# Optimization experiments

Measured on AMD Instinct MI355X. Metric: run time of the kernel, lower is better.

## Reference

```python
import jax, jax.numpy as jnp
import numpy as np

SR = 44100.0
BS, NT, SEQ = 2, 16, 262144
REV_N, TAPS = 65536, 1023

EQ_R = [(-12., 12.), (20., 2000.), (0.1, 5.0),
        (-12., 12.), (80., 2000.), (0.1, 5.0),
        (-12., 12.), (2000., 8000.), (0.1, 5.0),
        (-12., 12.), (8000., 12000.), (0.1, 5.0),
        (-12., 12.), (12000., 21050.), (0.1, 5.0),
        (-12., 12.), (6000., 21050.), (0.1, 5.0)]
COMP_R = [(-60., 0.), (1., 10.), (5., 250.), (10., 250.), (3., 12.), (0., 6.)]
TRACK_R = np.array([(-48., 48.)] + EQ_R + COMP_R + [(-80., 12.), (0., 1.)], np.float32)
MASTER_R = np.array([(-48., 48.)] + EQ_R + COMP_R + [(-48., 48.)], np.float32)


def _pow2(n):
    return 1 << int(np.ceil(np.log2(n)))


def _denorm(p, r):
    lo = jnp.asarray(r[:, 0])
    hi = jnp.asarray(r[:, 1])
    return p * (hi - lo) + lo


def _biquad(g_db, fc, q, ftype):
    # RBJ cookbook biquads, coefficients normalized by a0
    A = 10.0 ** (g_db / 40.0)
    w0 = 2.0 * np.pi * (fc / SR)
    al = jnp.sin(w0) / (2.0 * q)
    c = jnp.cos(w0)
    sA = jnp.sqrt(A)
    if ftype == 'low_shelf':
        b0 = A * ((A + 1) - (A - 1) * c + 2 * sA * al)
        b1 = 2 * A * ((A - 1) - (A + 1) * c)
        b2 = A * ((A + 1) - (A - 1) * c - 2 * sA * al)
        a0 = (A + 1) + (A - 1) * c + 2 * sA * al
        a1 = -2 * ((A - 1) + (A + 1) * c)
        a2 = (A + 1) + (A - 1) * c - 2 * sA * al
    elif ftype == 'high_shelf':
        b0 = A * ((A + 1) + (A - 1) * c + 2 * sA * al)
        b1 = -2 * A * ((A - 1) + (A + 1) * c)
        b2 = A * ((A + 1) + (A - 1) * c - 2 * sA * al)
        a0 = (A + 1) - (A - 1) * c + 2 * sA * al
        a1 = 2 * ((A - 1) - (A + 1) * c)
        a2 = (A + 1) - (A - 1) * c - 2 * sA * al
    else:  # peaking
        b0 = 1 + al * A
        b1 = -2 * c
        b2 = 1 - al * A
        a0 = 1 + al / A
        a1 = -2 * c
        a2 = 1 - al / A
    b = jnp.stack([b0, b1, b2], -1) / a0[..., None]
    a = jnp.stack([a0, a1, a2], -1) / a0[..., None]
    return b, a


def _apply_eq(x, p):
    # 6-section cascaded biquad EQ applied via frequency sampling (as dasp_pytorch does).
    # x: (..., S); p: (..., 18) broadcastable with x's leading dims.
    S = x.shape[-1]
    nfft = _pow2(2 * S - 1)
    nf = nfft // 2 + 1
    w = jnp.arange(nf, dtype=jnp.float32) * (2.0 * np.pi / nfft)
    z1 = jnp.exp(-1j * w)
    z2 = z1 * z1
    H = jnp.ones((nf,), jnp.complex64)
    for k, ftype in enumerate(['low_shelf', 'peaking', 'peaking', 'peaking', 'peaking', 'high_shelf']):
        b, a = _biquad(p[..., 3 * k], p[..., 3 * k + 1], p[..., 3 * k + 2], ftype)
        num = b[..., 0:1] + b[..., 1:2] * z1 + b[..., 2:3] * z2
        den = a[..., 0:1] + a[..., 1:2] * z1 + a[..., 2:3] * z2
        H = H * (num / den)
    X = jnp.fft.rfft(x, nfft)
    return jnp.fft.irfft(X * H, nfft)[..., :S].astype(x.dtype)


def _apply_comp(x, p, lookahead):
    # soft-knee compressor; gain smoothed by one-pole (attack) via frequency sampling.
    S = x.shape[-1]
    nfft = _pow2(2 * S - 1)
    nf = nfft // 2 + 1
    th, ratio, at_ms, rel_ms, knee, makeup = [p[..., i:i + 1] for i in range(6)]
    x_db = 20.0 * jnp.log10(jnp.maximum(jnp.abs(x), 1e-8))
    d = x_db - th
    x_sc = jnp.where(2.0 * d < -knee, x_db,
                     jnp.where(2.0 * jnp.abs(d) <= knee,
                               x_db + (1.0 / ratio - 1.0) * (d + knee / 2.0) ** 2 / (2.0 * knee),
                               th + d / ratio))
    g_c = x_sc - x_db  # gain reduction in dB (<= 0)
    alpha = jnp.exp(-jnp.log(9.0) / (SR * at_ms * 1e-3))  # (..., 1)
    w = jnp.arange(nf, dtype=jnp.float32) * (2.0 * np.pi / nfft)
    H = (1.0 - alpha) / (1.0 - alpha * jnp.exp(-1j * w))
    g_s = jnp.fft.irfft(jnp.fft.rfft(g_c, nfft) * H, nfft)[..., :S]
    if lookahead > 0:
        tail = jnp.repeat(g_s[..., -1:], lookahead, axis=-1)
        g_s = jnp.concatenate([g_s[..., lookahead:], tail], axis=-1)
    return (x * 10.0 ** ((g_s + makeup) / 20.0)).astype(x.dtype)


def _reverb(x, noise, fb, gains, decays, mix):
    # noise-shaped reverberation: 12 octave-band filtered noise bursts with
    # exponential decays summed into an IR, FFT-convolved with x, wet/dry mix.
    S = x.shape[-1]
    nL = _pow2(REV_N + TAPS - 1)
    filt = jnp.fft.irfft(jnp.fft.rfft(noise, nL) * jnp.fft.rfft(fb, nL), nL)
    filt = filt[..., TAPS - 1:TAPS - 1 + REV_N]  # (bs, 2, 12, REV_N) 'valid' part
    t = jnp.linspace(0.0, 1.0, REV_N)
    dec = decays * 10.0 + 1.0  # (bs, 12)
    env = jnp.exp(-dec[:, None, :, None] * t)
    ir = (filt * env * gains[:, None, :, None]).mean(axis=2)  # (bs, 2, REV_N)
    n2 = _pow2(S + REV_N - 1)
    wet = jnp.fft.irfft(jnp.fft.rfft(x, n2) * jnp.fft.rfft(ir, n2), n2)[..., :S]
    m = mix[:, None, None]
    return (1.0 - m) * x + m * wet


def _firwin_lp(numtaps, fc, fs):
    n = np.arange(numtaps) - (numtaps - 1) / 2.0
    h = (2.0 * fc / fs) * np.sinc(2.0 * fc / fs * n)
    h = h * np.hamming(numtaps)
    return h / h.sum()


def _octave_fb():
    centers = [31.5, 63., 125., 250., 500., 1000., 2000., 4000., 8000., 16000.]
    nyq = SR / 2.0
    filts = [_firwin_lp(TAPS, 22.3, SR)]  # lowpass below lowest octave
    for fc in centers:
        f1 = fc / np.sqrt(2.0)
        f2 = min(fc * np.sqrt(2.0), 0.999 * nyq)
        filts.append(_firwin_lp(TAPS, f2, SR) - _firwin_lp(TAPS, f1, SR))
    hp = -_firwin_lp(TAPS, 18000.0, SR)
    hp[(TAPS - 1) // 2] += 1.0  # highpass = delta - lowpass
    filts.append(hp)
    return np.stack(filts).astype(np.float32)  # (12, TAPS)


def _forward(tracks, track_params, fx_bus_params, master_bus_params, reverb_noise, fb):
    tpd = _denorm(track_params, TRACK_R)    # (bs, NT, 27)
    mpd = _denorm(master_bus_params, MASTER_R)  # (bs, 26)
    fxp = fx_bus_params  # reverb ranges are (0,1): denorm is identity

    x = tracks * 10.0 ** (tpd[..., 0:1] / 20.0)          # input fader
    x = _apply_eq(x, tpd[..., 1:19])                      # 6-band parametric EQ
    x = _apply_comp(x, tpd[..., 19:25], 2048)             # compressor, lookahead 2048

    theta = tpd[..., 26] * (np.pi / 2)                    # constant-power panner
    gl = jnp.sqrt(((np.pi / 2) - theta) * (2.0 / np.pi) * jnp.cos(theta))
    gr = jnp.sqrt(theta * (2.0 / np.pi) * jnp.sin(theta))
    panned = jnp.stack([x * gl[..., None], x * gr[..., None]], axis=1)  # (bs, 2, NT, S)

    master = panned.sum(axis=2)                           # (bs, 2, S)
    send = 10.0 ** (tpd[..., 25] / 20.0)                  # fx bus sends
    fx_in = (panned * send[:, None, :, None]).sum(axis=2)
    master = master + _reverb(fx_in, reverb_noise, fb, fxp[:, :12], fxp[:, 12:24], fxp[:, 24])

    master = master * 10.0 ** (mpd[:, 0, None, None] / 20.0)   # master input fader
    master = _apply_eq(master, mpd[:, None, 1:19])
    master = _apply_comp(master, mpd[:, None, 19:25], 1024)
    master = master * 10.0 ** (mpd[:, 25, None, None] / 20.0)  # output fader
    return panned, master


def setup_inputs() -> dict:
    key = jax.random.key(0)
    k = jax.random.split(key, 5)
    tracks = 0.1 * jax.random.normal(k[0], (BS, NT, SEQ), jnp.float32)
    track_params = jax.random.uniform(k[1], (BS, NT, 27), jnp.float32)
    fx_bus_params = jax.random.uniform(k[2], (BS, 25), jnp.float32)
    master_bus_params = jax.random.uniform(k[3], (BS, 26), jnp.float32)
    reverb_noise = jax.random.normal(k[4], (BS, 2, 12, REV_N + TAPS - 1), jnp.float32)
    fb = jnp.asarray(_octave_fb())
    return {'tracks': tracks, 'track_params': track_params, 'fx_bus_params': fx_bus_params,
            'master_bus_params': master_bus_params, 'reverb_noise': reverb_noise, 'fb': fb}


def reference(tracks, track_params, fx_bus_params, master_bus_params, reverb_noise, fb):
    return _forward(tracks, track_params, fx_bus_params, master_bus_params, reverb_noise, fb)
```

## Files before the change

### kernel.cpp

```cpp
#include <hip/hip_runtime.h>

#define DEVFN __device__ __forceinline__

constexpr int SEQ = 262144;
constexpr int REV_N = 65536;
constexpr int TAPS = 1023;
constexpr int NOISE_LEN = REV_N + TAPS - 1;

constexpr int NS_T = 32, L_T = 128, C_T = 2048;
constexpr int NS_M = 4,  L_M = 64,  C_M = 4096;
constexpr int LA_T = 2048, LA_M = 1024;

constexpr int OUT_MASTER_OFF = 16777216;

constexpr int PADX = 65552;
constexpr int XBL  = 327744;
constexpr int IRPAD = 4096;
constexpr int IRL  = 73728;
constexpr int PADN = 2016;
constexpr int XNL  = 68640;
constexpr int FPAD = 2048;
constexpr int FBL  = 4160;

#define C_DB  0.16609640474436813f
#define C_LOG 6.0205999132796239f
#define PI_D  3.14159265358979323846

typedef __attribute__((ext_vector_type(8)))  short short8v;
typedef __attribute__((ext_vector_type(16))) float f32x16;

struct SigP {
  float g_in;
  float cb0[6], cb1[6], cb2[6], ca1[6], ca2[6];
  float alpha, oma;
  float th, invr, knee, makeup;
  float g_out;
  float gl, gr, send;
};

constexpr size_t OFF_X   = 0;
constexpr size_t OFF_Y   = 33554432;
constexpr size_t OFF_FX  = 67108864;
constexpr size_t OFF_M0  = 71303168;
constexpr size_t OFF_FILT = OFF_X;
constexpr size_t OFF_IR   = OFF_X + 12582912;
constexpr size_t OFF_XM   = OFF_X + 16777216;
constexpr size_t OFF_M1   = OFF_Y;
constexpr size_t OFF_WP   = OFF_Y + 4194304;
constexpr size_t OFF_XB   = OFF_WP + 16777216;
constexpr size_t OFF_IR2  = OFF_XB + (size_t)4*XBL*2;
constexpr size_t OFF_XBN  = 58720256;
constexpr size_t OFF_FBV  = 65536000;
constexpr size_t OFF_E12 = OFF_FX;
constexpr size_t OFF_I12 = OFF_FX + 3145728;
constexpr size_t OFF_E1  = OFF_FX + 6291456;
constexpr size_t OFF_I1  = OFF_FX + 6553600;
constexpr size_t OFF_GL  = 75497472;
constexpr size_t OFF_PT  = OFF_GL + 1024;
constexpr size_t OFF_PM  = OFF_PT + 32*sizeof(SigP);
constexpr size_t OFF_ALT = (OFF_PM + 4*sizeof(SigP) + 7) & ~(size_t)7;
constexpr size_t OFF_ALM = OFF_ALT + 32*8;
constexpr size_t OFF_AT  = (OFF_ALM + 4*8 + 15) & ~(size_t)15;
constexpr size_t OFF_AM  = OFF_AT + 18432;

DEVFN int pq(int i){ return i + ((i >> 5) << 2); }
DEVFN int pqb(int i){ return i + ((i >> 5) << 3); }

DEVFN unsigned short f2bf(float f){
  unsigned int u = __float_as_uint(f);
  unsigned int r = (u + 0x7fffu + ((u >> 16) & 1u)) >> 16;
  return (unsigned short)r;
}
DEVFN float bf2f(unsigned short h){ return __uint_as_float(((unsigned int)h) << 16); }

DEVFN double dn(float p, double lo, double hi){ return (double)p*(hi-lo)+lo; }

__device__ void mk_sig(const float* p, int L, bool is_master,
                       SigP* sp, float* Tf, double* aL)
{
  const double flo[6] = {20.,80.,2000.,8000.,12000.,6000.};
  const double fhi[6] = {2000.,2000.,8000.,12000.,21050.,21050.};
  double gdb = dn(p[0], -48., 48.);
  sp->g_in = (float)exp2(gdb * 0.16609640474436813);
  double db0[6],db1[6],db2[6],da1[6],da2[6];
  for (int k=0;k<6;k++){
    double g  = dn(p[1+3*k], -12., 12.);
    double fc = dn(p[2+3*k], flo[k], fhi[k]);
    double q  = dn(p[3+3*k], 0.1, 5.0);
    double A  = pow(10.0, g/40.0);
    double w0 = 2.0*PI_D*(fc/44100.0);
    double al = sin(w0)/(2.0*q), co = cos(w0), sA = sqrt(A);
    double b0,b1,b2,a0,a1,a2;
    if (k==0){
      b0 = A*((A+1.0) - (A-1.0)*co + 2.0*sA*al);
      b1 = 2.0*A*((A-1.0) - (A+1.0)*co);
      b2 = A*((A+1.0) - (A-1.0)*co - 2.0*sA*al);
      a0 = (A+1.0) + (A-1.0)*co + 2.0*sA*al;
      a1 = -2.0*((A-1.0) + (A+1.0)*co);
      a2 = (A+1.0) + (A-1.0)*co - 2.0*sA*al;
    } else if (k==5){
      b0 = A*((A+1.0) + (A-1.0)*co + 2.0*sA*al);
      b1 = -2.0*A*((A-1.0) + (A+1.0)*co);
      b2 = A*((A+1.0) + (A-1.0)*co - 2.0*sA*al);
      a0 = (A+1.0) - (A-1.0)*co + 2.0*sA*al;
      a1 = 2.0*((A-1.0) - (A+1.0)*co);
      a2 = (A+1.0) - (A-1.0)*co - 2.0*sA*al;
    } else {
      b0 = 1.0 + al*A; b1 = -2.0*co; b2 = 1.0 - al*A;
      a0 = 1.0 + al/A; a1 = -2.0*co; a2 = 1.0 - al/A;
    }
    double ia0 = 1.0/a0;
    db0[k]=b0*ia0; db1[k]=b1*ia0; db2[k]=b2*ia0; da1[k]=a1*ia0; da2[k]=a2*ia0;
    sp->cb0[k]=(float)db0[k]; sp->cb1[k]=(float)db1[k]; sp->cb2[k]=(float)db2[k];
    sp->ca1[k]=(float)da1[k]; sp->ca2[k]=(float)da2[k];
  }
  for (int i=0;i<12;i++){
    double st[12]; for (int r=0;r<12;r++) st[r]=0.0; st[i]=1.0;
    double ns[12];
    double yprev=0.0, pm1=0.0, pm2=0.0;
    for (int k=0;k<6;k++){
      double yk = db0[k]*yprev + db1[k]*pm1 + db2[k]*pm2 - da1[k]*st[2*k] - da2[k]*st[2*k+1];
      ns[2*k]=yk; ns[2*k+1]=st[2*k];
      pm1=st[2*k]; pm2=st[2*k+1];
      yprev=yk;
    }
    for (int r=0;r<12;r++) Tf[r*12+i]=(float)ns[r];
  }
  double th    = dn(p[19], -60., 0.);
  double ratio = dn(p[20], 1., 10.);
  double at    = dn(p[21], 5., 250.);
  double knee  = dn(p[23], 3., 12.);
  double mkup  = dn(p[24], 0., 6.);
  double alpha = exp(-log(9.0)/(44100.0*at*0.001));
  sp->alpha=(float)alpha; sp->oma=(float)(1.0-alpha);
  sp->th=(float)th; sp->invr=(float)(1.0/ratio); sp->knee=(float)knee; sp->makeup=(float)mkup;
  *aL = pow(alpha, (double)L);
  if (is_master){
    sp->g_out = (float)exp2(dn(p[25],-48.,48.)*0.16609640474436813);
    sp->gl=0.f; sp->gr=0.f; sp->send=0.f;
  } else {
    sp->g_out = 1.f;
    sp->send = (float)exp2(dn(p[25],-80.,12.)*0.16609640474436813);
    double th2 = dn(p[26],0.,1.)*(PI_D/2.0);
    sp->gl = (float)sqrt((PI_D/2.0-th2)*(2.0/PI_D)*cos(th2));
    sp->gr = (float)sqrt(th2*(2.0/PI_D)*sin(th2));
  }
}

__global__ __launch_bounds__(64) void k_params(const float* __restrict__ tp, const float* __restrict__ mp,
    SigP* Pt, SigP* Pm, float* AT, float* AM, double* aLt, double* aLm)
{
  int i = threadIdx.x;
  if (i < 32)       mk_sig(tp + i*27, L_T, false, &Pt[i], AT + i*144, &aLt[i]);
  else if (i < 36){ int j=i-32; mk_sig(mp + (j>>1)*26, L_M, true, &Pm[j], AM + j*144, &aLm[j]); }
}

__global__ __launch_bounds__(64) void k_power(float* __restrict__ Ab, int lg)
{
  __shared__ float Ma[144], Mb[144];
  int sig = blockIdx.x, t = threadIdx.x;
  float* A = Ab + (size_t)sig*144;
  for (int idx=t; idx<144; idx+=64) Ma[idx]=A[idx];
  __syncthreads();
  int cur=0;
  for (int j=0;j<lg;j++){
    const float* src = cur? Mb:Ma;
    float* dst = cur? Ma:Mb;
    for (int idx=t; idx<144; idx+=64){
      int r=idx/12, cc=idx-r*12;
      float v=0.f;
      #pragma unroll
      for (int m=0;m<12;m++) v = fmaf(src[r*12+m], src[m*12+cc], v);
      dst[idx]=v;
    }
    __syncthreads();
    cur^=1;
  }
  const float* fin = cur? Mb:Ma;
  for (int idx=t; idx<144; idx+=64) A[idx]=fin[idx];
}

DEVFN float comp_gc(float y, float th, float invr, float kn){
  float av  = fmaxf(fabsf(y), 1e-8f);
  float xdb = C_LOG * __builtin_log2f(av);
  float d   = xdb - th;
  float w = (2.f*d < -kn) ? 0.f
          : ((2.f*fabsf(d) <= kn) ? (d+0.5f*kn)*(d+0.5f*kn)/(2.f*kn) : d);
  return (invr-1.f)*w;
}

__global__ __launch_bounds__(256) void k_eqA12(const float* __restrict__ in, const SigP* __restrict__ P,
    float* __restrict__ E12, int C, int L)
{
  int tid = blockIdx.x*256 + threadIdx.x;
  int sig = tid / C, c = tid - sig*C;
  const SigP* sp = P + sig;
  float B0[6],B1[6],B2[6],A1[6],A2[6];
  float g = sp->g_in;
  #pragma unroll
  for (int k=0;k<6;k++){
    float gg = (k==0)? g : 1.f;
    B0[k]=sp->cb0[k]*gg; B1[k]=sp->cb1[k]*gg; B2[k]=sp->cb2[k]*gg;
    A1[k]=sp->ca1[k];    A2[k]=sp->ca2[k];
  }
  const float* xp = in + (size_t)sig*SEQ + (size_t)c*L;
  float xm1=0.f, xm2=0.f;
  if (c){ xm1=xp[-1]; xm2=xp[-2]; }
  float s[12];
  #pragma unroll
  for (int r=0;r<12;r++) s[r]=0.f;
  for (int i=0;i<L;i+=4){
    float4 v = *(const float4*)(xp+i);
    #pragma unroll
    for (int u4=0;u4<4;u4++){
      float u = (u4==0)?v.x:(u4==1)?v.y:(u4==2)?v.z:v.w;
      float yprev=u, pm1=xm1, pm2=xm2;
      float ny[6];
      #pragma unroll
      for (int k=0;k<6;k++){
        float t0 = fmaf(B0[k],yprev, fmaf(B1[k],pm1, fmaf(B2[k],pm2, -A2[k]*s[2*k+1])));
        float yk = fmaf(-A1[k], s[2*k], t0);
        ny[k]=yk;
        pm1=s[2*k]; pm2=s[2*k+1];
        yprev=yk;
      }
      #pragma unroll
      for (int k=0;k<6;k++){ s[2*k+1]=s[2*k]; s[2*k]=ny[k]; }
      xm2=xm1; xm1=u;
    }
  }
  float* ep = E12 + (size_t)tid*12;
  #pragma unroll
  for (int r=0;r<12;r++) ep[r]=s[r];
}

__global__ __launch_bounds__(64) void k_scan12(const float* __restrict__ E, float* __restrict__ I,
    const float* __restrict__ Ab, int C, int Q, int lgQ)
{
  __shared__ float As[144], Pa[144], Pb[144];
  __shared__ float seg[64][12], ini[64][12];
  __shared__ float scur[12], stmp[12];
  int sig = blockIdx.x, t = threadIdx.x;
  const float* Asig = Ab + (size_t)sig*144;
  for (int idx=t; idx<144; idx+=64) As[idx]=Asig[idx];
  __syncthreads();
  const float* dp = E + ((size_t)sig*C + (size_t)t*Q)*12;
  float s[12];
  #pragma unroll
  for (int r=0;r<12;r++) s[r]=0.f;
  for (int j=0;j<Q;j++){
    const float* d = dp + j*12;
    float ns[12];
    #pragma unroll
    for (int r=0;r<12;r++){
      float v = d[r];
      #pragma unroll
      for (int cc=0;cc<12;cc++) v = fmaf(As[r*12+cc], s[cc], v);
      ns[r]=v;
    }
    #pragma unroll
    for (int r=0;r<12;r++) s[r]=ns[r];
  }
  #pragma unroll
  for (int r=0;r<12;r++) seg[t][r]=s[r];
  for (int idx=t; idx<144; idx+=64) Pa[idx]=As[idx];
  __syncthreads();
  int cur=0;
  for (int j=0;j<lgQ;j++){
    const float* src = cur? Pb:Pa;
    float* dst = cur? Pa:Pb;
    for (int idx=t; idx<144; idx+=64){
      int r=idx/12, cc=idx-r*12;
      float v=0.f;
      #pragma unroll
      for (int m=0;m<12;m++) v = fmaf(src[r*12+m], src[m*12+cc], v);
      dst[idx]=v;
    }
    __syncthreads();
    cur^=1;
  }
  const float* AQ = cur? Pb:Pa;
  if (t<12) scur[t]=0.f;
  __syncthreads();
  for (int u=0;u<64;u++){
    if (t<12){
      ini[u][t]=scur[t];
      float v = seg[u][t];
      #pragma unroll
      for (int cc=0;cc<12;cc++) v = fmaf(AQ[t*12+cc], scur[cc], v);
      stmp[t]=v;
    }
    __syncthreads();
    if (t<12) scur[t]=stmp[t];
    __syncthreads();
  }
  #pragma unroll
  for (int r=0;r<12;r++) s[r]=ini[t][r];
  float* op = I + ((size_t)sig*C + (size_t)t*Q)*12;
  for (int j=0;j<Q;j++){
    float* o = op + j*12;
    #pragma unroll
    for (int r=0;r<12;r++) o[r]=s[r];
    const float* d = dp + j*12;
    float ns[12];
    #pragma unroll
    for (int r=0;r<12;r++){
      float v = d[r];
      #pragma unroll
      for (int cc=0;cc<12;cc++) v = fmaf(As[r*12+cc], s[cc], v);
      ns[r]=v;
    }
    #pragma unroll
    for (int r=0;r<12;r++) s[r]=ns[r];
  }
}

__global__ __launch_bounds__(64) void k_scan1p(const float* __restrict__ endst, float* __restrict__ inits,
    const double* __restrict__ aL, int C, int Q, int lgQ)
{
  __shared__ double ag[64], ins[64];
  int sig = blockIdx.x; int t = threadIdx.x;
  double a = aL[sig];
  const float* dp = endst + (size_t)sig*C + (size_t)t*Q;
  double e=0.0;
  for (int j=0;j<Q;j++) e = a*e + (double)dp[j];
  ag[t]=e;
  __syncthreads();
  if (t == 0){
    double p=a;
    for (int j=0;j<lgQ;j++) p = p*p;
    double s=0.0;
    for (int u=0;u<64;u++){
      ins[u]=s;
      s = p*s + ag[u];
    }
  }
  __syncthreads();
  double s = ins[t];
  float* op = inits + (size_t)sig*C + (size_t)t*Q;
  for (int j=0;j<Q;j++){ op[j]=(float)s; s = a*s + (double)dp[j]; }
}

__global__ __launch_bounds__(256) void k_eqC12(const float* __restrict__ in, float* __restrict__ yout,
    const SigP* __restrict__ P, const float* __restrict__ I12, float* __restrict__ E1, int C, int L)
{
  int tid = blockIdx.x*256 + threadIdx.x;
  int sig = tid / C, c = tid - sig*C;
  const SigP* sp = P + sig;
  float B0[6],B1[6],B2[6],A1[6],A2[6];
  float g = sp->g_in;
  #pragma unroll
  for (int k=0;k<6;k++){
    float gg = (k==0)? g : 1.f;
    B0[k]=sp->cb0[k]*gg; B1[k]=sp->cb1[k]*gg; B2[k]=sp->cb2[k]*gg;
    A1[k]=sp->ca1[k];    A2[k]=sp->ca2[k];
  }
  float al=sp->alpha, oma=sp->oma, th=sp->th, invr=sp->invr, kn=sp->knee;
  size_t base = (size_t)sig*SEQ + (size_t)c*L;
  const float* xp = in + base;
  float* op = yout + base;
  float xm1=0.f, xm2=0.f;
  if (c){ xm1=xp[-1]; xm2=xp[-2]; }
  const float* ip = I12 + (size_t)tid*12;
  float s[12];
  #pragma unroll
  for (int r=0;r<12;r++) s[r]=ip[r];
  float gacc=0.f;
  for (int i=0;i<L;i+=4){
    float4 v = *(const float4*)(xp+i);
    float4 o;
    #pragma unroll
    for (int u4=0;u4<4;u4++){
      float u = (u4==0)?v.x:(u4==1)?v.y:(u4==2)?v.z:v.w;
      float yprev=u, pm1=xm1, pm2=xm2;
      float ny[6];
      #pragma unroll
      for (int k=0;k<6;k++){
        float t0 = fmaf(B0[k],yprev, fmaf(B1[k],pm1, fmaf(B2[k],pm2, -A2[k]*s[2*k+1])));
        float yk = fmaf(-A1[k], s[2*k], t0);
        ny[k]=yk;
        pm1=s[2*k]; pm2=s[2*k+1];
        yprev=yk;
      }
      #pragma unroll
      for (int k=0;k<6;k++){ s[2*k+1]=s[2*k]; s[2*k]=ny[k]; }
      xm2=xm1; xm1=u;
      float y5 = ny[5];
      if (u4==0) o.x=y5; else if (u4==1) o.y=y5; else if (u4==2) o.z=y5; else o.w=y5;
      gacc = fmaf(al, gacc, oma*comp_gc(y5,th,invr,kn));
    }
    *(float4*)(op+i) = o;
  }
  E1[tid]=gacc;
}

__global__ __launch_bounds__(256) void k_smoothcomp(const float* __restrict__ yin,
    const SigP* __restrict__ P, const float* __restrict__ inits1, float* __restrict__ gslast,
    float* __restrict__ outp, int C, int L, int lac)
{
  int tid = blockIdx.x*256 + threadIdx.x;
  int sig = tid / C, c = tid - sig*C;
  const SigP* sp = P + sig;
  float al=sp->alpha, oma=sp->oma, th=sp->th, invr=sp->invr, kn=sp->knee;
  float mk=sp->makeup, go=sp->g_out;
  size_t base = (size_t)sig*SEQ + (size_t)c*L;
  const float* xp = yin + base;
  bool wr = (c >= lac);
  size_t ob = wr ? (base - (size_t)lac*L) : 0;
  const float* yp = yin + ob;
  float* op = outp + ob;
  float gsv = inits1[tid];
  for (int i=0;i<L;i+=4){
    float4 v = *(const float4*)(xp+i);
    float4 gf;
    gsv = fmaf(al, gsv, oma*comp_gc(v.x,th,invr,kn)); gf.x=gsv;
    gsv = fmaf(al, gsv, oma*comp_gc(v.y,th,invr,kn)); gf.y=gsv;
    gsv = fmaf(al, gsv, oma*comp_gc(v.z,th,invr,kn)); gf.z=gsv;
    gsv = fmaf(al, gsv, oma*comp_gc(v.w,th,invr,kn)); gf.w=gsv;
    if (wr){
      float4 y2 = *(const float4*)(yp+i);
      float4 o;
      o.x = y2.x * __builtin_exp2f((gf.x+mk)*C_DB) * go;
      o.y = y2.y * __builtin_exp2f((gf.y+mk)*C_DB) * go;
      o.z = y2.z * __builtin_exp2f((gf.z+mk)*C_DB) * go;
      o.w = y2.w * __builtin_exp2f((gf.w+mk)*C_DB) * go;
      *(float4*)(op+i) = o;
    }
  }
  if (c == C-1) gslast[sig] = gsv;
}

__global__ __launch_bounds__(256) void k_comptail(const float* __restrict__ yin, const float* __restrict__ gslast,
    const SigP* __restrict__ P, float* __restrict__ outp, int la)
{
  int q = blockIdx.x*256 + threadIdx.x;
  int per = la/4;
  int sig = q / per;
  int r = (q - sig*per)*4;
  int n = SEQ - la + r;
  const SigP* sp = P + sig;
  float f = __builtin_exp2f((gslast[sig]+sp->makeup)*C_DB) * sp->g_out;
  size_t base = (size_t)sig*SEQ + n;
  float4 v = *(const float4*)(yin+base);
  float4 o = { v.x*f, v.y*f, v.z*f, v.w*f };
  *(float4*)(outp+base) = o;
}

__global__ __launch_bounds__(256) void k_pan(const float* __restrict__ y, const SigP* __restrict__ P,
    float* __restrict__ panned, float* __restrict__ m0, float* __restrict__ fx)
{
  int q = blockIdx.x*256 + threadIdx.x;
  int b = q / (SEQ/4);
  int n = (q - b*(SEQ/4))*4;
  float4 aL={0,0,0,0}, aR={0,0,0,0}, fL={0,0,0,0}, fR={0,0,0,0};
  for (int t=0;t<16;t++){
    const SigP* sp = P + b*16 + t;
    float gl=sp->gl, gr=sp->gr, sd=sp->send;
    float4 v = *(const float4*)(y + (size_t)(b*16+t)*SEQ + n);
    float4 pl = { v.x*gl, v.y*gl, v.z*gl, v.w*gl };
    float4 pr = { v.x*gr, v.y*gr, v.z*gr, v.w*gr };
    *(float4*)(panned + (size_t)(b*32+t)*SEQ + n)    = pl;
    *(float4*)(panned + (size_t)(b*32+16+t)*SEQ + n) = pr;
    aL.x+=pl.x; aL.y+=pl.y; aL.z+=pl.z; aL.w+=pl.w;
    aR.x+=pr.x; aR.y+=pr.y; aR.z+=pr.z; aR.w+=pr.w;
    fL.x=fmaf(pl.x,sd,fL.x); fL.y=fmaf(pl.y,sd,fL.y); fL.z=fmaf(pl.z,sd,fL.z); fL.w=fmaf(pl.w,sd,fL.w);
    fR.x=fmaf(pr.x,sd,fR.x); fR.y=fmaf(pr.y,sd,fR.y); fR.z=fmaf(pr.z,sd,fR.z); fR.w=fmaf(pr.w,sd,fR.w);
  }
  *(float4*)(m0 + (size_t)(b*2+0)*SEQ + n) = aL;
  *(float4*)(m0 + (size_t)(b*2+1)*SEQ + n) = aR;
  *(float4*)(fx + (size_t)(b*2+0)*SEQ + n) = fL;
  *(float4*)(fx + (size_t)(b*2+1)*SEQ + n) = fR;
}

__global__ __launch_bounds__(256) void k_ir(const float* __restrict__ filt, const float* __restrict__ fxp,
    float* __restrict__ ir)
{
  int q = blockIdx.x*256 + threadIdx.x;
  int sig = q / (REV_N/4);
  int i   = (q - sig*(REV_N/4))*4;
  int b = sig >> 1;
  float4 acc={0,0,0,0};
  const float ts = 1.0f/65535.0f;
  for (int band=0; band<12; band++){
    float gn  = fxp[b*25 + band];
    float dec = fxp[b*25 + 12 + band]*10.f + 1.f;
    float4 f = *(const float4*)(filt + ((size_t)(sig*12+band))*REV_N + i);
    float s = -dec*ts;
    float e0=expf(s*(float)i), e1=expf(s*(float)(i+1)), e2=expf(s*(float)(i+2)), e3=expf(s*(float)(i+3));
    acc.x = fmaf(gn*e0, f.x, acc.x);
    acc.y = fmaf(gn*e1, f.y, acc.y);
    acc.z = fmaf(gn*e2, f.z, acc.z);
    acc.w = fmaf(gn*e3, f.w, acc.w);
  }
  const float inv12 = 1.f/12.f;
  acc.x*=inv12; acc.y*=inv12; acc.z*=inv12; acc.w*=inv12;
  *(float4*)(ir + (size_t)sig*REV_N + i) = acc;
}

__global__ __launch_bounds__(256) void k_prepx(const float* __restrict__ fx, unsigned short* __restrict__ XB)
{
  int q = blockIdx.x*256 + threadIdx.x;
  int sig = q / XBL;
  int m   = q - sig*XBL;
  int a = m - PADX;
  float v = (a >= 0 && a < SEQ) ? fx[(size_t)sig*SEQ + a] : 0.f;
  XB[(size_t)sig*XBL + m] = f2bf(v);
}
__global__ __launch_bounds__(256) void k_prepir(const float* __restrict__ ir, unsigned short* __restrict__ IRV)
{
  int q = blockIdx.x*256 + threadIdx.x;
  int sig = q / IRL;
  int m   = q - sig*IRL;
  int a = m - IRPAD;
  float v = (a >= 0 && a < REV_N) ? ir[(size_t)sig*REV_N + (REV_N-1 - a)] : 0.f;
  IRV[(size_t)sig*IRL + m] = f2bf(v);
}
__global__ __launch_bounds__(256) void k_prepn(const float* __restrict__ noise, unsigned short* __restrict__ XBN)
{
  int q = blockIdx.x*256 + threadIdx.x;
  int sig = q / XNL;
  if (sig >= 48) return;
  int m   = q - sig*XNL;
  int a = m - PADN + 1022;
  float v = (a >= 0 && a < NOISE_LEN) ? noise[(size_t)sig*NOISE_LEN + a] : 0.f;
  XBN[(size_t)sig*XNL + m] = f2bf(v);
}
__global__ __launch_bounds__(256) void k_prepfb(const float* __restrict__ fb, unsigned short* __restrict__ FBV)
{
  int q = blockIdx.x*256 + threadIdx.x;
  int band = q / FBL;
  if (band >= 12) return;
  int m = q - band*FBL;
  int a = m - FPAD;
  float v = (a >= 0 && a < TAPS) ? fb[band*TAPS + (TAPS-1 - a)] : 0.f;
  FBV[(size_t)band*FBL + m] = f2bf(v);
}

__global__ __launch_bounds__(256,3) void k_firm(const unsigned short* __restrict__ XBN,
    const unsigned short* __restrict__ FBV, float* __restrict__ filt)
{
  __shared__ alignas(16) unsigned int xs0[4640];
  __shared__ alignas(16) unsigned int xs1[4640];
  __shared__ alignas(16) unsigned short sir[3840];
  int b = blockIdx.x;
  int ng  = b & 7;
  int sig = b >> 3;
  int band = sig % 12;
  int nblk = ng << 13;
  const int sbeg = -62;
  const int send = 126;

  int tid = threadIdx.x;
  int l  = tid & 63, wv = tid >> 6;
  int lj = l & 31, lg = l >> 5, ph = l & 1;
  int hl = (lj + 8*lg - ph) >> 1;
  int offB = 32*lj - 8*lg;
  const unsigned int* xbu = (const unsigned int*)(XBN + (size_t)sig*XNL);
  const unsigned short* irg = FBV + (size_t)band*FBL;
  const unsigned int* xsel = ph ? (const unsigned int*)xs1 : (const unsigned int*)xs0;

  f32x16 acc0 = {};
  f32x16 acc1 = {};
  int n0_0 = nblk + (wv*2+0)*1024;
  int n0_1 = nblk + (wv*2+1)*1024;

  for (int sa = sbeg; sa < send; sa += 128){
    int ns = send - sa; if (ns > 128) ns = 128;
    __syncthreads();
    int clo = nblk - 16*(sa + ns - 1);
    int ub  = (PADN + clo) >> 1;
    int nd  = ((nblk + 7168 + 46 - 16*sa) - clo)/2 + 2;
    for (int d = tid; d < nd; d += 256){
      unsigned int u0 = xbu[ub + d], u1 = xbu[ub + d + 1];
      xs0[d] = u0;
      xs1[d] = (u0 >> 16) | (u1 << 16);
    }
    int amin = 1022 - 16*(sa + ns - 1) - 992;
    int irlo = ((amin - 6) & ~7) + 6;
    int irspan = (1022 - 16*sa + 15) - irlo + 1;
    for (int r = tid; r < irspan; r += 256){
      sir[pqb(r)] = irg[FPAD + irlo + r];
    }
    __syncthreads();
    int db0 = ((n0_0 - clo) >> 1) - 8*sa + hl;
    int db1 = ((n0_1 - clo) >> 1) - 8*sa + hl;
    int Dh0 = 1022 - 16*sa - irlo;
    for (int ss = 0; ss < ns; ss++){
      int rB = (Dh0 - 16*ss) - offB;
      short8v bfrag = *(const short8v*)(sir + pqb(rB));
      union { unsigned int u[4]; short8v v; } a0, a1;
      int d0 = db0 - 8*ss, d1 = db1 - 8*ss;
      a0.u[0]=xsel[d0];   a0.u[1]=xsel[d0+1]; a0.u[2]=xsel[d0+2]; a0.u[3]=xsel[d0+3];
      a1.u[0]=xsel[d1];   a1.u[1]=xsel[d1+1]; a1.u[2]=xsel[d1+2]; a1.u[3]=xsel[d1+3];
      acc0 = __builtin_amdgcn_mfma_f32_32x32x16_bf16(a0.v, bfrag, acc0, 0, 0, 0);
      acc1 = __builtin_amdgcn_mfma_f32_32x32x16_bf16(a1.v, bfrag, acc1, 0, 0, 0);
    }
  }
  float* fp = filt + (size_t)sig*REV_N;
  #pragma unroll
  for (int reg = 0; reg < 16; reg++){
    int i = (reg & 3) + 8*(reg >> 2) + 4*lg;
    fp[n0_0 + i + 32*lj] = acc0[reg];
    fp[n0_1 + i + 32*lj] = acc1[reg];
  }
}

__global__ __launch_bounds__(256,2) void k_wetm(const unsigned short* __restrict__ XB,
    const unsigned short* __restrict__ IRV, unsigned short* __restrict__ WP)
{
  __shared__ alignas(16) unsigned int xs0[6688];
  __shared__ alignas(16) unsigned int xs1[6688];
  __shared__ alignas(16) unsigned short sir[6400];
  int b = blockIdx.x;
  int ng  = b & 15;
  int sig = (b >> 4) & 3;
  int kp  = b >> 6;
  int nblk = ng << 14;
  int sbeg = -254 + 544*kp;
  int send = sbeg + 544; if (send > 4097) send = 4097;

  int tid = threadIdx.x;
  int l  = tid & 63, wv = tid >> 6;
  int lj = l & 31, lg = l >> 5, ph = l & 1;
  int hl = (lj + 8*lg - ph) >> 1;
  int offB = 32*lj - 8*lg;
  const unsigned int* xbu = (const unsigned int*)(XB + (size_t)sig*XBL);
  const unsigned short* irg = IRV + (size_t)sig*IRL;
  const unsigned int* xsel = ph ? (const unsigned int*)xs1 : (const unsigned int*)xs0;

  f32x16 acc0 = {}, acc1 = {}, acc2 = {}, acc3 = {};
  int n0_w = nblk + wv*4096;

  for (int sa = sbeg; sa < send; sa += 64){
    int ns = send - sa; if (ns > 64) ns = 64;
    __syncthreads();
    int clo = nblk - 16*(sa + ns - 1);
    int ub  = (PADX + clo) >> 1;
    int nd  = (12336 + 16*(ns-1))/2 + 2;
    for (int d = tid; d < nd; d += 256){
      unsigned int u0 = xbu[ub + d], u1 = xbu[ub + d + 1];
      xs0[d] = u0;
      xs1[d] = (u0 >> 16) | (u1 << 16);
    }
    int amin = 65535 - 16*(sa + ns - 1) - 4064;
    int irlo = ((amin - 7) & ~7) + 7;
    int irspan = (65535 - 16*sa + 15) - irlo + 1;
    for (int r = tid; r < irspan; r += 256){
      sir[pqb(r)] = irg[IRPAD + irlo + r];
    }
    __syncthreads();
    int db0 = ((n0_w - clo) >> 1) - 8*sa + hl;
    int Dh0 = 65535 - 16*sa - irlo;
    for (int ss = 0; ss < ns; ss++){
      int rB = (Dh0 - 16*ss) - offB;
      int pb = pqb(rB);
      short8v bf0 = *(const short8v*)(sir + pb);
      short8v bf1 = *(const short8v*)(sir + pb - 1280);
      short8v bf2 = *(const short8v*)(sir + pb - 2560);
      short8v bf3 = *(const short8v*)(sir + pb - 3840);
      union { unsigned int u[4]; short8v v; } a0;
      int d0 = db0 - 8*ss;
      a0.u[0]=xsel[d0]; a0.u[1]=xsel[d0+1]; a0.u[2]=xsel[d0+2]; a0.u[3]=xsel[d0+3];
      acc0 = __builtin_amdgcn_mfma_f32_32x32x16_bf16(a0.v, bf0, acc0, 0, 0, 0);
      acc1 = __builtin_amdgcn_mfma_f32_32x32x16_bf16(a0.v, bf1, acc1, 0, 0, 0);
      acc2 = __builtin_amdgcn_mfma_f32_32x32x16_bf16(a0.v, bf2, acc2, 0, 0, 0);
      acc3 = __builtin_amdgcn_mfma_f32_32x32x16_bf16(a0.v, bf3, acc3, 0, 0, 0);
    }
  }
  unsigned short* wp = WP + ((size_t)(kp*4+sig))*SEQ;
  #pragma unroll
  for (int reg = 0; reg < 16; reg++){
    int i = (reg & 3) + 8*(reg >> 2) + 4*lg;
    int o = n0_w + i + 32*lj;
    wp[o]        = f2bf(acc0[reg]);
    wp[o + 1024] = f2bf(acc1[reg]);
    wp[o + 2048] = f2bf(acc2[reg]);
    wp[o + 3072] = f2bf(acc3[reg]);
  }
}

__global__ __launch_bounds__(256) void k_wetred(const unsigned short* __restrict__ wp, const float* __restrict__ fx,
    const float* __restrict__ m0, const float* __restrict__ fxp, float* __restrict__ m1)
{
  int q = blockIdx.x*256 + threadIdx.x;
  int sig = q / (SEQ/4);
  int n = (q - sig*(SEQ/4))*4;
  float mix = fxp[(sig>>1)*25+24];
  size_t ob = (size_t)sig*SEQ + n;
  float s0=0.f, s1=0.f, s2=0.f, s3=0.f;
  #pragma unroll
  for (int kp=0; kp<8; kp++){
    const unsigned short* p = wp + ((size_t)(kp*4+sig))*SEQ + n;
    s0 += bf2f(p[0]); s1 += bf2f(p[1]); s2 += bf2f(p[2]); s3 += bf2f(p[3]);
  }
  float4 w0 = *(const float4*)(m0+ob);
  float4 x0 = *(const float4*)(fx+ob);
  float om = 1.f - mix;
  float4 o;
  o.x = w0.x + om*x0.x + mix*s0;
  o.y = w0.y + om*x0.y + mix*s1;
  o.z = w0.z + om*x0.z + mix*s2;
  o.w = w0.w + om*x0.w + mix*s3;
  *(float4*)(m1+ob) = o;
}

extern "C" void kernel_launch(void* const* d_in, const int* in_sizes, int n_in,
                              void* d_out, int out_size, void* d_ws, size_t ws_size,
                              hipStream_t stream)
{
  const float* tracks = (const float*)d_in[0];
  const float* tp     = (const float*)d_in[1];
  const float* fxp    = (const float*)d_in[2];
  const float* mp     = (const float*)d_in[3];
  const float* noise  = (const float*)d_in[4];
  const float* fbp    = (const float*)d_in[5];
  float* out = (float*)d_out;
  char* w = (char*)d_ws;

  float*  X   = (float*)(w + OFF_X);
  float*  Y   = (float*)(w + OFF_Y);
  float*  FXb = (float*)(w + OFF_FX);
  float*  M0  = (float*)(w + OFF_M0);
  float*  E12 = (float*)(w + OFF_E12);
  float*  I12 = (float*)(w + OFF_I12);
  float*  E1  = (float*)(w + OFF_E1);
  float*  I1  = (float*)(w + OFF_I1);
  float*  GLt = (float*)(w + OFF_GL);
  float*  GLm = GLt + 32;
  SigP*   Pt  = (SigP*)(w + OFF_PT);
  SigP*   Pm  = (SigP*)(w + OFF_PM);
  double* aLt = (double*)(w + OFF_ALT);
  double* aLm = (double*)(w + OFF_ALM);
  float*  AT  = (float*)(w + OFF_AT);
  float*  AM  = (float*)(w + OFF_AM);
  float*  FILT= (float*)(w + OFF_FILT);
  float*  IR  = (float*)(w + OFF_IR);
  float*  XM  = (float*)(w + OFF_XM);
  float*  M1  = (float*)(w + OFF_M1);
  unsigned short* WPu = (unsigned short*)(w + OFF_WP);
  unsigned short* XB  = (unsigned short*)(w + OFF_XB);
  unsigned short* IRV = (unsigned short*)(w + OFF_IR2);
  unsigned short* XBN = (unsigned short*)(w + OFF_XBN);
  unsigned short* FBV = (unsigned short*)(w + OFF_FBV);

  k_params<<<1,64,0,stream>>>(tp, mp, Pt, Pm, AT, AM, aLt, aLm);
  k_power<<<32,64,0,stream>>>(AT, 7);
  k_power<<<4,64,0,stream>>>(AM, 6);

  const int GT = NS_T*C_T/256;
  k_eqA12<<<GT,256,0,stream>>>(tracks, Pt, E12, C_T, L_T);
  k_scan12<<<NS_T,64,0,stream>>>(E12, I12, AT, C_T, C_T/64, 5);
  k_eqC12<<<GT,256,0,stream>>>(tracks, Y, Pt, I12, E1, C_T, L_T);
  k_scan1p<<<NS_T,64,0,stream>>>(E1, I1, aLt, C_T, C_T/64, 5);
  k_smoothcomp<<<GT,256,0,stream>>>(Y, Pt, I1, GLt, X, C_T, L_T, LA_T/L_T);
  k_comptail<<<NS_T*(LA_T/4)/256,256,0,stream>>>(Y, GLt, Pt, X, LA_T);
  k_pan<<<2*(SEQ/4)/256,256,0,stream>>>(X, Pt, out, M0, FXb);

  k_prepn<<<(48*XNL+255)/256,256,0,stream>>>(noise, XBN);
  k_prepfb<<<(12*FBL+255)/256,256,0,stream>>>(fbp, FBV);
  k_firm<<<384,256,0,stream>>>(XBN, FBV, FILT);
  k_ir<<<4*(REV_N/4)/256,256,0,stream>>>(FILT, fxp, IR);
  k_prepx<<<(4*XBL)/256,256,0,stream>>>(FXb, XB);
  k_prepir<<<(4*IRL)/256,256,0,stream>>>(IR, IRV);
  k_wetm<<<512,256,0,stream>>>(XB, IRV, WPu);
  k_wetred<<<4*(SEQ/4)/256,256,0,stream>>>(WPu, FXb, M0, fxp, M1);

  const int GM = NS_M*C_M/256;
  k_eqA12<<<GM,256,0,stream>>>(M1, Pm, E12, C_M, L_M);
  k_scan12<<<NS_M,64,0,stream>>>(E12, I12, AM, C_M, C_M/64, 6);
  k_eqC12<<<GM,256,0,stream>>>(M1, XM, Pm, I12, E1, C_M, L_M);
  k_scan1p<<<NS_M,64,0,stream>>>(E1, I1, aLm, C_M, C_M/64, 6);
  k_smoothcomp<<<GM,256,0,stream>>>(XM, Pm, I1, GLm, out + OUT_MASTER_OFF, C_M, L_M, LA_M/L_M);
  k_comptail<<<NS_M*(LA_M/4)/256,256,0,stream>>>(XM, GLm, Pm, out + OUT_MASTER_OFF, LA_M);
}
```

Before: 509.7 us.

## Merge prep and power kernels, fuse IR bf16 conversion, double wet-conv staging chunk

Merges the two matrix-power launches into one, folds the three bf16 prep kernels for fx, noise and filterbank into a single launch, and has the IR kernel write the reversed bf16 IR with its zero padding directly. Together these drop several launches and one full pass over the IR. The reverb convolution kernel now stages 128 shifts per shared-memory chunk instead of 64, which halves the sync and reload count. In exchange it uses more LDS per block, which may reduce occupancy below the requested two blocks per CU.

Result: faster. 493.0 us (-3.3%).

```diff
diff --git a/kernel.cpp b/kernel.cpp
--- a/kernel.cpp
+++ b/kernel.cpp
@@ -155,11 +155,13 @@
   else if (i < 36){ int j=i-32; mk_sig(mp + (j>>1)*26, L_M, true, &Pm[j], AM + j*144, &aLm[j]); }
 }
 
-__global__ __launch_bounds__(64) void k_power(float* __restrict__ Ab, int lg)
+__global__ __launch_bounds__(64) void k_power2(float* __restrict__ AT, float* __restrict__ AM)
 {
   __shared__ float Ma[144], Mb[144];
-  int sig = blockIdx.x, t = threadIdx.x;
-  float* A = Ab + (size_t)sig*144;
+  int b = blockIdx.x, t = threadIdx.x;
+  float* A; int lg;
+  if (b < 32){ A = AT + (size_t)b*144; lg = 7; }
+  else       { A = AM + (size_t)(b-32)*144; lg = 6; }
   for (int idx=t; idx<144; idx+=64) Ma[idx]=A[idx];
   __syncthreads();
   int cur=0;
@@ -472,12 +474,13 @@
   *(float4*)(fx + (size_t)(b*2+1)*SEQ + n) = fR;
 }
 
-__global__ __launch_bounds__(256) void k_ir(const float* __restrict__ filt, const float* __restrict__ fxp,
-    float* __restrict__ ir)
+__global__ __launch_bounds__(256) void k_ir2(const float* __restrict__ filt, const float* __restrict__ fxp,
+    float* __restrict__ ir, unsigned short* __restrict__ IRV)
 {
   int q = blockIdx.x*256 + threadIdx.x;
   int sig = q / (REV_N/4);
-  int i   = (q - sig*(REV_N/4))*4;
+  int idx = q - sig*(REV_N/4);
+  int i   = idx*4;
   int b = sig >> 1;
   float4 acc={0,0,0,0};
   const float ts = 1.0f/65535.0f;
@@ -495,45 +498,48 @@
   const float inv12 = 1.f/12.f;
   acc.x*=inv12; acc.y*=inv12; acc.z*=inv12; acc.w*=inv12;
   *(float4*)(ir + (size_t)sig*REV_N + i) = acc;
-}
-
-__global__ __launch_bounds__(256) void k_prepx(const float* __restrict__ fx, unsigned short* __restrict__ XB)
+  unsigned short* iv = IRV + (size_t)sig*IRL;
+  int base = IRPAD + REV_N-1 - i;
+  iv[base]   = f2bf(acc.x);
+  iv[base-1] = f2bf(acc.y);
+  iv[base-2] = f2bf(acc.z);
+  iv[base-3] = f2bf(acc.w);
+  if (idx < 1024){
+    *(ushort4*)(iv + idx*4) = make_ushort4(0,0,0,0);
+  } else if (idx < 2048){
+    *(ushort4*)(iv + IRPAD + REV_N + (idx-1024)*4) = make_ushort4(0,0,0,0);
+  }
+}
+
+constexpr int P3_XB  = 4*XBL;
+constexpr int P3_XBN = 48*XNL;
+constexpr int P3_TOT = P3_XB + P3_XBN + 12*FBL;
+__global__ __launch_bounds__(256) void k_prep3(const float* __restrict__ fx, const float* __restrict__ noise,
+    const float* __restrict__ fb, unsigned short* __restrict__ XB, unsigned short* __restrict__ XBN,
+    unsigned short* __restrict__ FBV)
 {
   int q = blockIdx.x*256 + threadIdx.x;
-  int sig = q / XBL;
-  int m   = q - sig*XBL;
-  int a = m - PADX;
-  float v = (a >= 0 && a < SEQ) ? fx[(size_t)sig*SEQ + a] : 0.f;
-  XB[(size_t)sig*XBL + m] = f2bf(v);
-}
-__global__ __launch_bounds__(256) void k_prepir(const float* __restrict__ ir, unsigned short* __restrict__ IRV)
-{
-  int q = blockIdx.x*256 + threadIdx.x;
-  int sig = q / IRL;
-  int m   = q - sig*IRL;
-  int a = m - IRPAD;
-  float v = (a >= 0 && a < REV_N) ? ir[(size_t)sig*REV_N + (REV_N-1 - a)] : 0.f;
-  IRV[(size_t)sig*IRL + m] = f2bf(v);
-}
-__global__ __launch_bounds__(256) void k_prepn(const float* __restrict__ noise, unsigned short* __restrict__ XBN)
-{
-  int q = blockIdx.x*256 + threadIdx.x;
-  int sig = q / XNL;
-  if (sig >= 48) return;
-  int m   = q - sig*XNL;
-  int a = m - PADN + 1022;
-  float v = (a >= 0 && a < NOISE_LEN) ? noise[(size_t)sig*NOISE_LEN + a] : 0.f;
-  XBN[(size_t)sig*XNL + m] = f2bf(v);
-}
-__global__ __launch_bounds__(256) void k_prepfb(const float* __restrict__ fb, unsigned short* __restrict__ FBV)
-{
-  int q = blockIdx.x*256 + threadIdx.x;
-  int band = q / FBL;
-  if (band >= 12) return;
-  int m = q - band*FBL;
-  int a = m - FPAD;
-  float v = (a >= 0 && a < TAPS) ? fb[band*TAPS + (TAPS-1 - a)] : 0.f;
-  FBV[(size_t)band*FBL + m] = f2bf(v);
+  if (q < P3_XB){
+    int sig = q / XBL;
+    int m   = q - sig*XBL;
+    int a = m - PADX;
+    float v = (a >= 0 && a < SEQ) ? fx[(size_t)sig*SEQ + a] : 0.f;
+    XB[(size_t)sig*XBL + m] = f2bf(v);
+  } else if (q < P3_XB + P3_XBN){
+    int q2 = q - P3_XB;
+    int sig = q2 / XNL;
+    int m   = q2 - sig*XNL;
+    int a = m - PADN + 1022;
+    float v = (a >= 0 && a < NOISE_LEN) ? noise[(size_t)sig*NOISE_LEN + a] : 0.f;
+    XBN[(size_t)sig*XNL + m] = f2bf(v);
+  } else if (q < P3_TOT){
+    int q3 = q - P3_XB - P3_XBN;
+    int band = q3 / FBL;
+    int m = q3 - band*FBL;
+    int a = m - FPAD;
+    float v = (a >= 0 && a < TAPS) ? fb[band*TAPS + (TAPS-1 - a)] : 0.f;
+    FBV[(size_t)band*FBL + m] = f2bf(v);
+  }
 }
 
 __global__ __launch_bounds__(256,3) void k_firm(const unsigned short* __restrict__ XBN,
@@ -608,9 +614,9 @@
 __global__ __launch_bounds__(256,2) void k_wetm(const unsigned short* __restrict__ XB,
     const unsigned short* __restrict__ IRV, unsigned short* __restrict__ WP)
 {
-  __shared__ alignas(16) unsigned int xs0[6688];
-  __shared__ alignas(16) unsigned int xs1[6688];
-  __shared__ alignas(16) unsigned short sir[6400];
+  __shared__ alignas(16) unsigned int xs0[7200];
+  __shared__ alignas(16) unsigned int xs1[7200];
+  __shared__ alignas(16) unsigned short sir[7680];
   int b = blockIdx.x;
   int ng  = b & 15;
   int sig = (b >> 4) & 3;
@@ -631,8 +637,8 @@
   f32x16 acc0 = {}, acc1 = {}, acc2 = {}, acc3 = {};
   int n0_w = nblk + wv*4096;
 
-  for (int sa = sbeg; sa < send; sa += 64){
-    int ns = send - sa; if (ns > 64) ns = 64;
+  for (int sa = sbeg; sa < send; sa += 128){
+    int ns = send - sa; if (ns > 128) ns = 128;
     __syncthreads();
     int clo = nblk - 16*(sa + ns - 1);
     int ub  = (PADX + clo) >> 1;
@@ -744,8 +750,7 @@
   unsigned short* FBV = (unsigned short*)(w + OFF_FBV);
 
   k_params<<<1,64,0,stream>>>(tp, mp, Pt, Pm, AT, AM, aLt, aLm);
-  k_power<<<32,64,0,stream>>>(AT, 7);
-  k_power<<<4,64,0,stream>>>(AM, 6);
+  k_power2<<<36,64,0,stream>>>(AT, AM);
 
   const int GT = NS_T*C_T/256;
   k_eqA12<<<GT,256,0,stream>>>(tracks, Pt, E12, C_T, L_T);
@@ -756,12 +761,9 @@
   k_comptail<<<NS_T*(LA_T/4)/256,256,0,stream>>>(Y, GLt, Pt, X, LA_T);
   k_pan<<<2*(SEQ/4)/256,256,0,stream>>>(X, Pt, out, M0, FXb);
 
-  k_prepn<<<(48*XNL+255)/256,256,0,stream>>>(noise, XBN);
-  k_prepfb<<<(12*FBL+255)/256,256,0,stream>>>(fbp, FBV);
+  k_prep3<<<(P3_TOT+255)/256,256,0,stream>>>(FXb, noise, fbp, XB, XBN, FBV);
   k_firm<<<384,256,0,stream>>>(XBN, FBV, FILT);
-  k_ir<<<4*(REV_N/4)/256,256,0,stream>>>(FILT, fxp, IR);
-  k_prepx<<<(4*XBL)/256,256,0,stream>>>(FXb, XB);
-  k_prepir<<<(4*IRL)/256,256,0,stream>>>(IR, IRV);
+  k_ir2<<<4*(REV_N/4)/256,256,0,stream>>>(FILT, fxp, IR, IRV);
   k_wetm<<<512,256,0,stream>>>(XB, IRV, WPu);
   k_wetred<<<4*(SEQ/4)/256,256,0,stream>>>(WPu, FXb, M0, fxp, M1);
 
```
